# Kernel optimization log

Measured on AMD Instinct MI355X. Metric: run time of the kernel, lower is better.

The kernel has to match this reference:

```python
import jax, jax.numpy as jnp
import numpy as np

B, C, H, W = 4, 512, 64, 64
C8 = C // 8  # 64
COUT = 512

def conv1x1(x, w, b=None):
    # x: (B,C,H,W), w: (O,C) -> (B,O,H,W)
    y = jnp.einsum('bchw,oc->bohw', x, w)
    if b is not None:
        y = y + b[None, :, None, None]
    return y

def setup_inputs() -> dict:
    key = jax.random.key(0)
    ks = jax.random.split(key, 10)
    s = 0.02
    x  = jax.random.normal(ks[0], (B, C, H, W), dtype=jnp.float32)
    Wq = jax.random.normal(ks[1], (C8, C), dtype=jnp.float32) * s
    bq = jnp.zeros((C8,), dtype=jnp.float32)
    Wk = jax.random.normal(ks[2], (C8, C), dtype=jnp.float32) * s
    bk = jnp.zeros((C8,), dtype=jnp.float32)
    Wv = jax.random.normal(ks[3], (C, C), dtype=jnp.float32) * s
    bv = jnp.zeros((C,), dtype=jnp.float32)
    gamma = jax.random.normal(ks[4], (1,), dtype=jnp.float32)  # torch init is 0; random for nontrivial grads
    Wd = jax.random.normal(ks[5], (COUT, C), dtype=jnp.float32) * s
    bd = jnp.zeros((COUT,), dtype=jnp.float32)
    return {"x": x, "Wq": Wq, "bq": bq, "Wk": Wk, "bk": bk,
            "Wv": Wv, "bv": bv, "gamma": gamma, "Wd": Wd, "bd": bd}

def reference(x, Wq, bq, Wk, bk, Wv, bv, gamma, Wd, bd):
    b, c, h, w = x.shape
    hw = h * w
    q = conv1x1(x, Wq, bq).reshape(b, C8, hw)   # (B,C8,HW)
    k = conv1x1(x, Wk, bk).reshape(b, C8, hw)   # (B,C8,HW)
    v = conv1x1(x, Wv, bv).reshape(b, c, hw)    # (B,C,HW)
    # energy[b,i,j] = q[:, :, i] . k[:, :, j]  (no scaling, as in source)
    energy = jnp.einsum('bci,bcj->bij', q, k)   # (B,HW,HW)
    attention = jax.nn.softmax(energy, axis=-1)
    # out[b,c,i] = sum_j v[b,c,j] * attention[b,i,j]
    out = jnp.einsum('bcj,bij->bci', v, attention).reshape(b, c, h, w)
    out = gamma[0] * out + x
    pam_out = conv1x1(out, Wd, bd)              # layer4: 1x1 conv to 512
    return pam_out
```

## Files before the change

### kernel.cpp

```cpp
#include <hip/hip_runtime.h>
#include <stdint.h>

#define HW   4096
#define CIN  512

typedef __attribute__((ext_vector_type(8))) short short8;
typedef __attribute__((ext_vector_type(4))) float f32x4;
typedef unsigned short u16;

#define GL16(src, ldsdst) __builtin_amdgcn_global_load_lds(                    \
    (const __attribute__((address_space(1))) void*)(src),                      \
    (__attribute__((address_space(3))) void*)(ldsdst), 16, 0, 0)

__device__ __forceinline__ u16 f2bf(float f) {
  union { float f; uint32_t u; } c; c.f = f;
  uint32_t r = (c.u + 0x7FFFu + ((c.u >> 16) & 1u)) >> 16;
  return (u16)r;
}
__device__ __forceinline__ float bf2f(u16 h) {
  union { uint32_t u; float f; } c; c.u = ((uint32_t)h) << 16;
  return c.f;
}

__global__ __launch_bounds__(256) void cast_xT(const float* __restrict__ x,
                                               u16* __restrict__ xbT) {
  __shared__ u16 t[64 * 72];
  int p0 = blockIdx.x * 64, c0 = blockIdx.y * 64, b = blockIdx.z;
  int tid = threadIdx.x, r = tid >> 2, ch = tid & 3;
  const float* xp = x + ((size_t)b * CIN + c0 + r) * HW + p0 + ch * 16;
  float4 f0 = *(const float4*)(xp + 0);
  float4 f1 = *(const float4*)(xp + 4);
  float4 f2 = *(const float4*)(xp + 8);
  float4 f3 = *(const float4*)(xp + 12);
  u16* tr = &t[r * 72 + ch * 16];
  tr[0] = f2bf(f0.x); tr[1] = f2bf(f0.y); tr[2] = f2bf(f0.z); tr[3] = f2bf(f0.w);
  tr[4] = f2bf(f1.x); tr[5] = f2bf(f1.y); tr[6] = f2bf(f1.z); tr[7] = f2bf(f1.w);
  tr[8] = f2bf(f2.x); tr[9] = f2bf(f2.y); tr[10] = f2bf(f2.z); tr[11] = f2bf(f2.w);
  tr[12] = f2bf(f3.x); tr[13] = f2bf(f3.y); tr[14] = f2bf(f3.z); tr[15] = f2bf(f3.w);
  __syncthreads();
  u16 o[16];
#pragma unroll
  for (int j = 0; j < 16; j++) o[j] = t[(ch * 16 + j) * 72 + r];
  u16* op = xbT + ((size_t)b * HW + p0 + r) * CIN + c0 + ch * 16;
  *(short8*)(op) = *(short8*)&o[0];
  *(short8*)(op + 8) = *(short8*)&o[8];
}

__global__ void cast_w(const float* __restrict__ Wq, const float* __restrict__ Wk,
                       const float* __restrict__ Wv, const float* __restrict__ Wd,
                       const float* __restrict__ bq, const float* __restrict__ bk,
                       u16* __restrict__ wqk, u16* __restrict__ wv,
                       u16* __restrict__ wd, float* __restrict__ bqk) {
  const float LOG2E = 1.4426950408889634f;
  int i = blockIdx.x * 256 + threadIdx.x;
  if (i < 65536) wqk[i] = f2bf(i < 32768 ? Wq[i] * LOG2E : Wk[i - 32768]);
  if (i < 262144) { wv[i] = f2bf(Wv[i]); wd[i] = f2bf(Wd[i]); }
  if (i < 128) bqk[i] = (i < 64) ? bq[i] * LOG2E : bk[i - 64];
}

__global__ __launch_bounds__(256) void gemm_bf16(
    const u16* __restrict__ A, const u16* __restrict__ BT,
    const float* __restrict__ bias, void* __restrict__ out,
    int M, int N, int K, int mode) {
  __shared__ u16 la[128 * 32];
  __shared__ u16 lb[128 * 32];
  int tid = threadIdx.x;
  int w = tid >> 6, lane = tid & 63, m = lane & 15, g = lane >> 4;
  int wm = w >> 1, wn = w & 1;
  int m0 = blockIdx.y * 128, n0 = blockIdx.x * 128;
  int sr = lane >> 2, sc = (lane & 3) * 8;
  const u16* pa0 = A + (size_t)(m0 + w * 32 + sr) * K + sc;
  const u16* pa1 = pa0 + (size_t)16 * K;
  const u16* pb0 = BT + (size_t)(n0 + w * 32 + sr) * K + sc;
  const u16* pb1 = pb0 + (size_t)16 * K;
  u16* la0 = &la[(w * 32) * 32];
  u16* la1 = &la[(w * 32 + 16) * 32];
  u16* lb0 = &lb[(w * 32) * 32];
  u16* lb1 = &lb[(w * 32 + 16) * 32];

  f32x4 acc[4][4];
  f32x4 zero = {0.f, 0.f, 0.f, 0.f};
#pragma unroll
  for (int i = 0; i < 4; i++)
#pragma unroll
    for (int j = 0; j < 4; j++) acc[i][j] = zero;

  for (int k0 = 0; k0 < K; k0 += 32) {
    __syncthreads();
    GL16(pa0 + k0, la0);
    GL16(pa1 + k0, la1);
    GL16(pb0 + k0, lb0);
    GL16(pb1 + k0, lb1);
    __syncthreads();
    short8 af[4], bf[4];
#pragma unroll
    for (int i = 0; i < 4; i++)
      af[i] = *(const short8*)&la[(wm * 64 + i * 16 + m) * 32 + g * 8];
#pragma unroll
    for (int j = 0; j < 4; j++)
      bf[j] = *(const short8*)&lb[(wn * 64 + j * 16 + m) * 32 + g * 8];
#pragma unroll
    for (int i = 0; i < 4; i++)
#pragma unroll
      for (int j = 0; j < 4; j++)
        acc[i][j] = __builtin_amdgcn_mfma_f32_16x16x32_bf16(af[i], bf[j], acc[i][j], 0, 0, 0);
  }

#pragma unroll
  for (int i = 0; i < 4; i++) {
#pragma unroll
    for (int j = 0; j < 4; j++) {
      int row_l = m0 + wm * 64 + i * 16 + g * 4;
      int col = n0 + wn * 64 + j * 16 + m;
#pragma unroll
      for (int r = 0; r < 4; r++) {
        int row = row_l + r;
        float v = acc[i][j][r];
        if (mode == 0) {
          v += bias[col];
          ((u16*)out)[(size_t)row * N + col] = f2bf(v);
        } else {
          v += bias[row];
          size_t addr = ((size_t)(col >> 12) * M + row) * HW + (col & (HW - 1));
          if (mode == 1) ((u16*)out)[addr] = f2bf(v);
          else           ((float*)out)[addr] = v;
        }
      }
    }
  }
}

__global__ __launch_bounds__(512) void ppass(
    const u16* __restrict__ qkT, u16* __restrict__ P,
    float* __restrict__ li, int b0) {
  __shared__ u16 kl[256 * 64];
  __shared__ float red[2][64];
  int tid = threadIdx.x;
  int w = tid >> 6, lane = tid & 63, m = lane & 15, g = lane >> 4;
  int blk = blockIdx.x;
  int bb = blk >> 6, b = b0 + bb;
  int q0 = (blk & 63) << 6;
  int qg = w & 3, jh = w >> 2;
  size_t qrow = (size_t)b * HW + q0;

  short8 aq[2];
#pragma unroll
  for (int ks = 0; ks < 2; ks++)
    aq[ks] = *(const short8*)(qkT + (qrow + qg * 16 + m) * 128 + ks * 32 + g * 8);

  float lr[4] = {0.f, 0.f, 0.f, 0.f};
  u16* Pb = P + ((size_t)bb * HW + q0) * HW;
  const u16* kb = qkT + (size_t)b * HW * 128 + 64;
  f32x4 zero = {0.f, 0.f, 0.f, 0.f};

  for (int jp = 0; jp < 16; jp++) {
    int j0 = jp * 256;
    __syncthreads();
#pragma unroll
    for (int it = 0; it < 4; it++) {
      int c = tid + it * 512;
      int row = c >> 3, seg = c & 7;
      short8 v = *(const short8*)(kb + (size_t)(j0 + row) * 128 + seg * 8);
      *(short8*)&kl[row * 64 + ((seg ^ (row & 7)) * 8)] = v;
    }
    __syncthreads();
#pragma unroll
    for (int jt = 0; jt < 8; jt++) {
      int jr = jh * 128 + jt * 16;
      int krow = jr + m;
      f32x4 s = zero;
#pragma unroll
      for (int ks = 0; ks < 2; ks++) {
        short8 bk = *(const short8*)&kl[krow * 64 + (((ks * 4 + g) ^ (krow & 7)) * 8)];
        s = __builtin_amdgcn_mfma_f32_16x16x32_bf16(aq[ks], bk, s, 0, 0, 0);
      }
      int j = j0 + jr + m;
#pragma unroll
      for (int r = 0; r < 4; r++) {
        float p = exp2f(s[r]);
        lr[r] += p;
        Pb[(size_t)(qg * 16 + g * 4 + r) * HW + j] = f2bf(p);
      }
    }
  }
#pragma unroll
  for (int r = 0; r < 4; r++) {
#pragma unroll
    for (int off = 1; off < 16; off <<= 1)
      lr[r] += __shfl_xor(lr[r], off);
  }
  __syncthreads();
  if (m == 0) {
#pragma unroll
    for (int r = 0; r < 4; r++) red[jh][qg * 16 + g * 4 + r] = lr[r];
  }
  __syncthreads();
  if (tid < 64) li[qrow + tid] = 1.0f / (red[0][tid] + red[1][tid]);
}

__global__ __launch_bounds__(256) void gemm_pv(
    const u16* __restrict__ P, const u16* __restrict__ V,
    const float* __restrict__ li, const u16* __restrict__ xbT,
    const float* __restrict__ gamma, u16* __restrict__ uT, int b0) {
  __shared__ u16 la[4][128 * 32];
  __shared__ u16 lb[4][128 * 32];
  int tid = threadIdx.x;
  int w = tid >> 6, lane = tid & 63, m = lane & 15, g = lane >> 4;
  int wm = w >> 1, wn = w & 1;
  int total = gridDim.x * gridDim.y * gridDim.z;
  int lid = blockIdx.x + (blockIdx.y << 2) + (blockIdx.z << 7);
  int wk = (lid & 7) * (total >> 3) + (lid >> 3);
  int chan = (wk & 3) << 7;
  int q0 = ((wk >> 2) & 31) << 7;
  int bb = wk >> 7, b = b0 + bb;
  int sr = lane >> 2, sc = (lane & 3) * 8;

  const u16* pa0 = P + ((size_t)bb * HW + q0 + w * 32 + sr) * HW + sc;
  const u16* pa1 = pa0 + (size_t)16 * HW;
  const u16* pb0 = V + ((size_t)b * CIN + chan + w * 32 + sr) * HW + sc;
  const u16* pb1 = pb0 + (size_t)16 * HW;

  f32x4 acc[4][4];
  f32x4 zero = {0.f, 0.f, 0.f, 0.f};
#pragma unroll
  for (int i = 0; i < 4; i++)
#pragma unroll
    for (int j = 0; j < 4; j++) acc[i][j] = zero;

  for (int k0 = 0; k0 < HW; k0 += 128) {
    __syncthreads();
#pragma unroll
    for (int c = 0; c < 4; c++) {
      int kk = k0 + c * 32;
      GL16(pa0 + kk, &la[c][(w * 32) * 32]);
      GL16(pa1 + kk, &la[c][(w * 32 + 16) * 32]);
      GL16(pb0 + kk, &lb[c][(w * 32) * 32]);
      GL16(pb1 + kk, &lb[c][(w * 32 + 16) * 32]);
    }
    __syncthreads();
#pragma unroll
    for (int c = 0; c < 4; c++) {
      short8 af[4], bf[4];
#pragma unroll
      for (int i = 0; i < 4; i++)
        af[i] = *(const short8*)&la[c][(wm * 64 + i * 16 + m) * 32 + g * 8];
#pragma unroll
      for (int j = 0; j < 4; j++)
        bf[j] = *(const short8*)&lb[c][(wn * 64 + j * 16 + m) * 32 + g * 8];
#pragma unroll
      for (int i = 0; i < 4; i++)
#pragma unroll
        for (int j = 0; j < 4; j++)
          acc[i][j] = __builtin_amdgcn_mfma_f32_16x16x32_bf16(af[i], bf[j], acc[i][j], 0, 0, 0);
    }
  }

  float gm = gamma[0];
#pragma unroll
  for (int i = 0; i < 4; i++) {
#pragma unroll
    for (int j = 0; j < 4; j++) {
#pragma unroll
      for (int r = 0; r < 4; r++) {
        int q = q0 + wm * 64 + i * 16 + g * 4 + r;
        int c = chan + wn * 64 + j * 16 + m;
        size_t row = (size_t)b * HW + q;
        float o = acc[i][j][r] * li[row];
        float xv = bf2f(xbT[row * CIN + c]);
        uT[row * CIN + c] = f2bf(gm * o + xv);
      }
    }
  }
}

extern "C" void kernel_launch(void* const* d_in, const int* in_sizes, int n_in,
                              void* d_out, int out_size, void* d_ws, size_t ws_size,
                              hipStream_t stream) {
  const float* x     = (const float*)d_in[0];
  const float* Wq    = (const float*)d_in[1];
  const float* bq    = (const float*)d_in[2];
  const float* Wk    = (const float*)d_in[3];
  const float* bk    = (const float*)d_in[4];
  const float* Wv    = (const float*)d_in[5];
  const float* bv    = (const float*)d_in[6];
  const float* gamma = (const float*)d_in[7];
  const float* Wd    = (const float*)d_in[8];
  const float* bd    = (const float*)d_in[9];

  char* ws = (char*)d_ws;
  size_t off = 0;
  auto alloc = [&](size_t bytes) {
    void* p = ws + off;
    off += (bytes + 255) & ~(size_t)255;
    return p;
  };
  u16*   xbT = (u16*)alloc((size_t)16384 * 512 * 2);
  u16*   qkT = (u16*)alloc((size_t)16384 * 128 * 2);
  u16*   vb  = (u16*)alloc((size_t)16384 * 512 * 2);
  u16*   uT  = (u16*)alloc((size_t)16384 * 512 * 2);
  u16*   wqk = (u16*)alloc((size_t)65536 * 2);
  u16*   wvb = (u16*)alloc((size_t)262144 * 2);
  u16*   wdb = (u16*)alloc((size_t)262144 * 2);
  float* bqk = (float*)alloc(128 * 4);
  float* li  = (float*)alloc((size_t)16384 * 4);
  size_t PB = (size_t)HW * HW * 2;
  int nb = 0;
  if      (off + 4 * PB <= ws_size) nb = 4;
  else if (off + 2 * PB <= ws_size) nb = 2;
  else if (off + 1 * PB <= ws_size) nb = 1;
  if (nb == 0) return;
  u16* Pbuf = (u16*)alloc(nb * PB);

  cast_xT<<<dim3(64, 8, 4), 256, 0, stream>>>(x, xbT);
  cast_w<<<1024, 256, 0, stream>>>(Wq, Wk, Wv, Wd, bq, bk, wqk, wvb, wdb, bqk);
  gemm_bf16<<<dim3(1, 128), 256, 0, stream>>>(xbT, wqk, bqk, qkT, 16384, 128, 512, 0);
  gemm_bf16<<<dim3(128, 4), 256, 0, stream>>>(wvb, xbT, bv, vb, 512, 16384, 512, 1);
  for (int b0 = 0; b0 < 4; b0 += nb) {
    ppass<<<dim3(nb * 64), 512, 0, stream>>>(qkT, Pbuf, li, b0);
    gemm_pv<<<dim3(4, 32, nb), 256, 0, stream>>>(Pbuf, vb, li, xbT, gamma, uT, b0);
  }
  gemm_bf16<<<dim3(128, 4), 256, 0, stream>>>(wdb, uT, bd, d_out, 512, 16384, 512, 2);
}
```

Measured before the change: 203.9 us.

## Deepen GEMM K-staging to 128 and halve ppass query tile for more blocks

```diff
diff --git a/kernel.cpp b/kernel.cpp
--- a/kernel.cpp
+++ b/kernel.cpp
@@ -62,8 +62,8 @@
     const u16* __restrict__ A, const u16* __restrict__ BT,
     const float* __restrict__ bias, void* __restrict__ out,
     int M, int N, int K, int mode) {
-  __shared__ u16 la[128 * 32];
-  __shared__ u16 lb[128 * 32];
+  __shared__ u16 la[4][128 * 32];
+  __shared__ u16 lb[4][128 * 32];
   int tid = threadIdx.x;
   int w = tid >> 6, lane = tid & 63, m = lane & 15, g = lane >> 4;
   int wm = w >> 1, wn = w & 1;
@@ -73,10 +73,6 @@
   const u16* pa1 = pa0 + (size_t)16 * K;
   const u16* pb0 = BT + (size_t)(n0 + w * 32 + sr) * K + sc;
   const u16* pb1 = pb0 + (size_t)16 * K;
-  u16* la0 = &la[(w * 32) * 32];
-  u16* la1 = &la[(w * 32 + 16) * 32];
-  u16* lb0 = &lb[(w * 32) * 32];
-  u16* lb1 = &lb[(w * 32 + 16) * 32];
 
   f32x4 acc[4][4];
   f32x4 zero = {0.f, 0.f, 0.f, 0.f};
@@ -85,25 +81,32 @@
 #pragma unroll
     for (int j = 0; j < 4; j++) acc[i][j] = zero;
 
-  for (int k0 = 0; k0 < K; k0 += 32) {
-    __syncthreads();
-    GL16(pa0 + k0, la0);
-    GL16(pa1 + k0, la1);
-    GL16(pb0 + k0, lb0);
-    GL16(pb1 + k0, lb1);
-    __syncthreads();
-    short8 af[4], bf[4];
-#pragma unroll
-    for (int i = 0; i < 4; i++)
-      af[i] = *(const short8*)&la[(wm * 64 + i * 16 + m) * 32 + g * 8];
-#pragma unroll
-    for (int j = 0; j < 4; j++)
-      bf[j] = *(const short8*)&lb[(wn * 64 + j * 16 + m) * 32 + g * 8];
-#pragma unroll
-    for (int i = 0; i < 4; i++)
+  for (int k0 = 0; k0 < K; k0 += 128) {
+    __syncthreads();
+#pragma unroll
+    for (int c = 0; c < 4; c++) {
+      int kk = k0 + c * 32;
+      GL16(pa0 + kk, &la[c][(w * 32) * 32]);
+      GL16(pa1 + kk, &la[c][(w * 32 + 16) * 32]);
+      GL16(pb0 + kk, &lb[c][(w * 32) * 32]);
+      GL16(pb1 + kk, &lb[c][(w * 32 + 16) * 32]);
+    }
+    __syncthreads();
+#pragma unroll
+    for (int c = 0; c < 4; c++) {
+      short8 af[4], bf[4];
+#pragma unroll
+      for (int i = 0; i < 4; i++)
+        af[i] = *(const short8*)&la[c][(wm * 64 + i * 16 + m) * 32 + g * 8];
 #pragma unroll
       for (int j = 0; j < 4; j++)
-        acc[i][j] = __builtin_amdgcn_mfma_f32_16x16x32_bf16(af[i], bf[j], acc[i][j], 0, 0, 0);
+        bf[j] = *(const short8*)&lb[c][(wn * 64 + j * 16 + m) * 32 + g * 8];
+#pragma unroll
+      for (int i = 0; i < 4; i++)
+#pragma unroll
+        for (int j = 0; j < 4; j++)
+          acc[i][j] = __builtin_amdgcn_mfma_f32_16x16x32_bf16(af[i], bf[j], acc[i][j], 0, 0, 0);
+    }
   }
 
 #pragma unroll
@@ -134,13 +137,13 @@
     const u16* __restrict__ qkT, u16* __restrict__ P,
     float* __restrict__ li, int b0) {
   __shared__ u16 kl[256 * 64];
-  __shared__ float red[2][64];
+  __shared__ float red[4][32];
   int tid = threadIdx.x;
   int w = tid >> 6, lane = tid & 63, m = lane & 15, g = lane >> 4;
   int blk = blockIdx.x;
-  int bb = blk >> 6, b = b0 + bb;
-  int q0 = (blk & 63) << 6;
-  int qg = w & 3, jh = w >> 2;
+  int bb = blk >> 7, b = b0 + bb;
+  int q0 = (blk & 127) << 5;
+  int qg = w & 1, jh = w >> 1;
   size_t qrow = (size_t)b * HW + q0;
 
   short8 aq[2];
@@ -165,8 +168,8 @@
     }
     __syncthreads();
 #pragma unroll
-    for (int jt = 0; jt < 8; jt++) {
-      int jr = jh * 128 + jt * 16;
+    for (int jt = 0; jt < 4; jt++) {
+      int jr = jh * 64 + jt * 16;
       int krow = jr + m;
       f32x4 s = zero;
 #pragma unroll
@@ -195,7 +198,8 @@
     for (int r = 0; r < 4; r++) red[jh][qg * 16 + g * 4 + r] = lr[r];
   }
   __syncthreads();
-  if (tid < 64) li[qrow + tid] = 1.0f / (red[0][tid] + red[1][tid]);
+  if (tid < 32)
+    li[qrow + tid] = 1.0f / (red[0][tid] + red[1][tid] + red[2][tid] + red[3][tid]);
 }
 
 __global__ __launch_bounds__(256) void gemm_pv(
@@ -316,7 +320,7 @@
   gemm_bf16<<<dim3(1, 128), 256, 0, stream>>>(xbT, wqk, bqk, qkT, 16384, 128, 512, 0);
   gemm_bf16<<<dim3(128, 4), 256, 0, stream>>>(wvb, xbT, bv, vb, 512, 16384, 512, 1);
   for (int b0 = 0; b0 < 4; b0 += nb) {
-    ppass<<<dim3(nb * 64), 512, 0, stream>>>(qkT, Pbuf, li, b0);
+    ppass<<<dim3(nb * 128), 512, 0, stream>>>(qkT, Pbuf, li, b0);
     gemm_pv<<<dim3(4, 32, nb), 256, 0, stream>>>(Pbuf, vb, li, xbT, gamma, uT, b0);
   }
   gemm_bf16<<<dim3(128, 4), 256, 0, stream>>>(wdb, uT, bd, d_out, 512, 16384, 512, 2);
```

Result: faster. 193.6 us (-5.1%).
